# Performance work log

Hardware: AMD Instinct MI355X
Metric: run time of the kernel (lower is better)

## Reference

```python
import jax, jax.numpy as jnp
import numpy as np

EPS = 1e-07

def setup_inputs() -> dict:
    key = jax.random.key(0)
    k1, k2 = jax.random.split(key)
    B, C = 65536, 1000
    output = jax.random.normal(k1, (B, C), dtype=jnp.float32)
    target = jax.random.randint(k2, (B,), 0, C, dtype=jnp.int64)
    return {"output": output, "target": target}

def reference(output, target):
    B, C = output.shape
    # L2-normalize each row (p=2 norm over class dim) then softmax over classes
    norms = jnp.linalg.norm(output, axis=-1, keepdims=True) + EPS
    probs = jax.nn.softmax(output / norms, axis=1)  # [B, C]
    # per-class mean confidence [C]
    avg_conf = jnp.mean(probs, axis=0)
    # per-class empirical frequency [C] via one-hot-free bincount
    counts = jnp.zeros((C,), dtype=probs.dtype).at[target].add(1.0)
    avg_count = counts / B
    # mean absolute calibration gap over classes (scalar)
    return jnp.mean(jnp.abs(avg_conf - avg_count))
```

## Files before the change

kernel.cpp:

```cpp
#include <hip/hip_runtime.h>
#include <math.h>

#define TPB 512
#define NBLK 1024
#define CCLS 1000

__global__ __launch_bounds__(TPB, 8) void mdca_main(const float* __restrict__ X,
                                                    float* __restrict__ g_acc, int B) {
  __shared__ float sacc[1024];
  const int t = threadIdx.x;
  const int lane = t & 63;
  const int wid = blockIdx.x * (TPB / 64) + (t >> 6);
  const int nw = NBLK * (TPB / 64);
  const bool v3 = (lane < 58);

  for (int i = t; i < 1024; i += TPB) sacc[i] = 0.f;

  float acc[16];
  #pragma unroll
  for (int i = 0; i < 16; ++i) acc[i] = 0.f;

  const float4 Z = make_float4(0.f, 0.f, 0.f, 0.f);

  for (int r0 = wid; r0 < B; r0 += 2 * nw) {
    const int r1 = r0 + nw;
    const bool has1 = (r1 < B);

    const float4* b0 = reinterpret_cast<const float4*>(X + (size_t)r0 * CCLS);
    const float4* b1 = reinterpret_cast<const float4*>(X + (size_t)(has1 ? r1 : r0) * CCLS);

    float4 a0 = b0[lane],       a1 = b0[64 + lane];
    float4 a2 = b0[128 + lane], a3 = v3 ? b0[192 + lane] : Z;
    float4 c0 = b1[lane],       c1 = b1[64 + lane];
    float4 c2 = b1[128 + lane], c3 = v3 ? b1[192 + lane] : Z;

    float ss0 = a0.x*a0.x + a0.y*a0.y + a0.z*a0.z + a0.w*a0.w
              + a1.x*a1.x + a1.y*a1.y + a1.z*a1.z + a1.w*a1.w
              + a2.x*a2.x + a2.y*a2.y + a2.z*a2.z + a2.w*a2.w
              + a3.x*a3.x + a3.y*a3.y + a3.z*a3.z + a3.w*a3.w;
    float ss1 = c0.x*c0.x + c0.y*c0.y + c0.z*c0.z + c0.w*c0.w
              + c1.x*c1.x + c1.y*c1.y + c1.z*c1.z + c1.w*c1.w
              + c2.x*c2.x + c2.y*c2.y + c2.z*c2.z + c2.w*c2.w
              + c3.x*c3.x + c3.y*c3.y + c3.z*c3.z + c3.w*c3.w;

    #pragma unroll
    for (int off = 1; off < 64; off <<= 1) {
      ss0 += __shfl_xor(ss0, off, 64);
      ss1 += __shfl_xor(ss1, off, 64);
    }

    const float inv0 = 1.0f / (sqrtf(ss0) + 1e-7f);
    const float inv1 = 1.0f / (sqrtf(ss1) + 1e-7f);

    float e0[16], e1[16];
    e0[0]=__expf(a0.x*inv0); e0[1]=__expf(a0.y*inv0); e0[2]=__expf(a0.z*inv0); e0[3]=__expf(a0.w*inv0);
    e0[4]=__expf(a1.x*inv0); e0[5]=__expf(a1.y*inv0); e0[6]=__expf(a1.z*inv0); e0[7]=__expf(a1.w*inv0);
    e0[8]=__expf(a2.x*inv0); e0[9]=__expf(a2.y*inv0); e0[10]=__expf(a2.z*inv0); e0[11]=__expf(a2.w*inv0);
    e1[0]=__expf(c0.x*inv1); e1[1]=__expf(c0.y*inv1); e1[2]=__expf(c0.z*inv1); e1[3]=__expf(c0.w*inv1);
    e1[4]=__expf(c1.x*inv1); e1[5]=__expf(c1.y*inv1); e1[6]=__expf(c1.z*inv1); e1[7]=__expf(c1.w*inv1);
    e1[8]=__expf(c2.x*inv1); e1[9]=__expf(c2.y*inv1); e1[10]=__expf(c2.z*inv1); e1[11]=__expf(c2.w*inv1);
    if (v3) {
      e0[12]=__expf(a3.x*inv0); e0[13]=__expf(a3.y*inv0); e0[14]=__expf(a3.z*inv0); e0[15]=__expf(a3.w*inv0);
      e1[12]=__expf(c3.x*inv1); e1[13]=__expf(c3.y*inv1); e1[14]=__expf(c3.z*inv1); e1[15]=__expf(c3.w*inv1);
    } else {
      e0[12]=e0[13]=e0[14]=e0[15]=0.f;
      e1[12]=e1[13]=e1[14]=e1[15]=0.f;
    }

    float es0 = 0.f, es1 = 0.f;
    #pragma unroll
    for (int i = 0; i < 16; ++i) { es0 += e0[i]; es1 += e1[i]; }
    #pragma unroll
    for (int off = 1; off < 64; off <<= 1) {
      es0 += __shfl_xor(es0, off, 64);
      es1 += __shfl_xor(es1, off, 64);
    }
    const float invS0 = 1.0f / es0;
    const float invS1 = has1 ? (1.0f / es1) : 0.f;

    #pragma unroll
    for (int i = 0; i < 16; ++i) acc[i] += e0[i] * invS0 + e1[i] * invS1;
  }

  __syncthreads();
  #pragma unroll
  for (int k = 0; k < 4; ++k)
    #pragma unroll
    for (int j = 0; j < 4; ++j)
      atomicAdd(&sacc[k * 256 + lane * 4 + j], acc[k * 4 + j]);
  __syncthreads();
  #pragma unroll
  for (int j = 0; j < 2; ++j) {
    int c = t * 2 + j;
    if (c < CCLS) atomicAdd(&g_acc[c], sacc[c]);
  }
}

__global__ __launch_bounds__(256) void mdca_count(const int* __restrict__ tgt,
                                                  float* __restrict__ g_cnt, int B) {
  __shared__ int scnt[CCLS];
  for (int i = threadIdx.x; i < CCLS; i += 256) scnt[i] = 0;
  __syncthreads();
  for (int i = blockIdx.x * 256 + threadIdx.x; i < B; i += gridDim.x * 256)
    atomicAdd(&scnt[tgt[i]], 1);
  __syncthreads();
  for (int i = threadIdx.x; i < CCLS; i += 256) {
    int v = scnt[i];
    if (v) atomicAdd(&g_cnt[i], (float)v);
  }
}

__global__ __launch_bounds__(256) void mdca_final(const float* __restrict__ g_acc,
                                                  const float* __restrict__ g_cnt,
                                                  float* __restrict__ out, int B) {
  __shared__ float s_r[4];
  int t = threadIdx.x;
  float invB = 1.0f / (float)B;
  float s = 0.f;
  for (int c = t; c < CCLS; c += 256)
    s += fabsf((g_acc[c] - g_cnt[c]) * invB);
  #pragma unroll
  for (int off = 32; off > 0; off >>= 1) s += __shfl_down(s, off, 64);
  if ((t & 63) == 0) s_r[t >> 6] = s;
  __syncthreads();
  if (t == 0) out[0] = (s_r[0] + s_r[1] + s_r[2] + s_r[3]) / (float)CCLS;
}

extern "C" void kernel_launch(void* const* d_in, const int* in_sizes, int n_in,
                              void* d_out, int out_size, void* d_ws, size_t ws_size,
                              hipStream_t stream) {
  const float* X = (const float*)d_in[0];
  const int* tgt = (const int*)d_in[1];
  const int B = in_sizes[1];

  float* g_acc = (float*)d_ws;
  float* g_cnt = g_acc + 1024;

  hipMemsetAsync(d_ws, 0, 2048 * sizeof(float), stream);

  mdca_main<<<NBLK, TPB, 0, stream>>>(X, g_acc, B);
  mdca_count<<<32, 256, 0, stream>>>(tgt, g_cnt, B);
  mdca_final<<<1, 256, 0, stream>>>(g_acc, g_cnt, (float*)d_out, B);
}
```

Before: 406.9 us.

## Replace global float atomics with per-block partials and parallel final reduction

```diff
diff --git a/kernel.cpp b/kernel.cpp
--- a/kernel.cpp
+++ b/kernel.cpp
@@ -6,7 +6,7 @@
 #define CCLS 1000
 
 __global__ __launch_bounds__(TPB, 8) void mdca_main(const float* __restrict__ X,
-                                                    float* __restrict__ g_acc, int B) {
+                                                    float* __restrict__ part, int B) {
   __shared__ float sacc[1024];
   const int t = threadIdx.x;
   const int lane = t & 63;
@@ -52,24 +52,20 @@
     const float inv0 = 1.0f / (sqrtf(ss0) + 1e-7f);
     const float inv1 = 1.0f / (sqrtf(ss1) + 1e-7f);
 
-    float e0[16], e1[16];
-    e0[0]=__expf(a0.x*inv0); e0[1]=__expf(a0.y*inv0); e0[2]=__expf(a0.z*inv0); e0[3]=__expf(a0.w*inv0);
-    e0[4]=__expf(a1.x*inv0); e0[5]=__expf(a1.y*inv0); e0[6]=__expf(a1.z*inv0); e0[7]=__expf(a1.w*inv0);
-    e0[8]=__expf(a2.x*inv0); e0[9]=__expf(a2.y*inv0); e0[10]=__expf(a2.z*inv0); e0[11]=__expf(a2.w*inv0);
-    e1[0]=__expf(c0.x*inv1); e1[1]=__expf(c0.y*inv1); e1[2]=__expf(c0.z*inv1); e1[3]=__expf(c0.w*inv1);
-    e1[4]=__expf(c1.x*inv1); e1[5]=__expf(c1.y*inv1); e1[6]=__expf(c1.z*inv1); e1[7]=__expf(c1.w*inv1);
-    e1[8]=__expf(c2.x*inv1); e1[9]=__expf(c2.y*inv1); e1[10]=__expf(c2.z*inv1); e1[11]=__expf(c2.w*inv1);
-    if (v3) {
-      e0[12]=__expf(a3.x*inv0); e0[13]=__expf(a3.y*inv0); e0[14]=__expf(a3.z*inv0); e0[15]=__expf(a3.w*inv0);
-      e1[12]=__expf(c3.x*inv1); e1[13]=__expf(c3.y*inv1); e1[14]=__expf(c3.z*inv1); e1[15]=__expf(c3.w*inv1);
-    } else {
-      e0[12]=e0[13]=e0[14]=e0[15]=0.f;
-      e1[12]=e1[13]=e1[14]=e1[15]=0.f;
-    }
+    a0.x=__expf(a0.x*inv0); a0.y=__expf(a0.y*inv0); a0.z=__expf(a0.z*inv0); a0.w=__expf(a0.w*inv0);
+    a1.x=__expf(a1.x*inv0); a1.y=__expf(a1.y*inv0); a1.z=__expf(a1.z*inv0); a1.w=__expf(a1.w*inv0);
+    a2.x=__expf(a2.x*inv0); a2.y=__expf(a2.y*inv0); a2.z=__expf(a2.z*inv0); a2.w=__expf(a2.w*inv0);
+    a3.x=__expf(a3.x*inv0); a3.y=__expf(a3.y*inv0); a3.z=__expf(a3.z*inv0); a3.w=__expf(a3.w*inv0);
+    c0.x=__expf(c0.x*inv1); c0.y=__expf(c0.y*inv1); c0.z=__expf(c0.z*inv1); c0.w=__expf(c0.w*inv1);
+    c1.x=__expf(c1.x*inv1); c1.y=__expf(c1.y*inv1); c1.z=__expf(c1.z*inv1); c1.w=__expf(c1.w*inv1);
+    c2.x=__expf(c2.x*inv1); c2.y=__expf(c2.y*inv1); c2.z=__expf(c2.z*inv1); c2.w=__expf(c2.w*inv1);
+    c3.x=__expf(c3.x*inv1); c3.y=__expf(c3.y*inv1); c3.z=__expf(c3.z*inv1); c3.w=__expf(c3.w*inv1);
+    if (!v3) { a3 = Z; c3 = Z; }
 
-    float es0 = 0.f, es1 = 0.f;
-    #pragma unroll
-    for (int i = 0; i < 16; ++i) { es0 += e0[i]; es1 += e1[i]; }
+    float es0 = a0.x+a0.y+a0.z+a0.w + a1.x+a1.y+a1.z+a1.w
+              + a2.x+a2.y+a2.z+a2.w + a3.x+a3.y+a3.z+a3.w;
+    float es1 = c0.x+c0.y+c0.z+c0.w + c1.x+c1.y+c1.z+c1.w
+              + c2.x+c2.y+c2.z+c2.w + c3.x+c3.y+c3.z+c3.w;
     #pragma unroll
     for (int off = 1; off < 64; off <<= 1) {
       es0 += __shfl_xor(es0, off, 64);
@@ -78,8 +74,14 @@
     const float invS0 = 1.0f / es0;
     const float invS1 = has1 ? (1.0f / es1) : 0.f;
 
-    #pragma unroll
-    for (int i = 0; i < 16; ++i) acc[i] += e0[i] * invS0 + e1[i] * invS1;
+    acc[0]  += a0.x*invS0 + c0.x*invS1;  acc[1]  += a0.y*invS0 + c0.y*invS1;
+    acc[2]  += a0.z*invS0 + c0.z*invS1;  acc[3]  += a0.w*invS0 + c0.w*invS1;
+    acc[4]  += a1.x*invS0 + c1.x*invS1;  acc[5]  += a1.y*invS0 + c1.y*invS1;
+    acc[6]  += a1.z*invS0 + c1.z*invS1;  acc[7]  += a1.w*invS0 + c1.w*invS1;
+    acc[8]  += a2.x*invS0 + c2.x*invS1;  acc[9]  += a2.y*invS0 + c2.y*invS1;
+    acc[10] += a2.z*invS0 + c2.z*invS1;  acc[11] += a2.w*invS0 + c2.w*invS1;
+    acc[12] += a3.x*invS0 + c3.x*invS1;  acc[13] += a3.y*invS0 + c3.y*invS1;
+    acc[14] += a3.z*invS0 + c3.z*invS1;  acc[15] += a3.w*invS0 + c3.w*invS1;
   }
 
   __syncthreads();
@@ -89,10 +91,9 @@
     for (int j = 0; j < 4; ++j)
       atomicAdd(&sacc[k * 256 + lane * 4 + j], acc[k * 4 + j]);
   __syncthreads();
-  #pragma unroll
-  for (int j = 0; j < 2; ++j) {
-    int c = t * 2 + j;
-    if (c < CCLS) atomicAdd(&g_acc[c], sacc[c]);
+  if (t < 256) {
+    float4 v = *reinterpret_cast<float4*>(&sacc[t * 4]);
+    *reinterpret_cast<float4*>(&part[(size_t)blockIdx.x * 1024 + t * 4]) = v;
   }
 }
 
@@ -110,20 +111,25 @@
   }
 }
 
-__global__ __launch_bounds__(256) void mdca_final(const float* __restrict__ g_acc,
-                                                  const float* __restrict__ g_cnt,
-                                                  float* __restrict__ out, int B) {
-  __shared__ float s_r[4];
-  int t = threadIdx.x;
-  float invB = 1.0f / (float)B;
+__global__ __launch_bounds__(64) void mdca_final(const float* __restrict__ part,
+                                                 const float* __restrict__ g_cnt,
+                                                 float* __restrict__ out, int B) {
+  const int c = blockIdx.x * 64 + threadIdx.x;
   float s = 0.f;
-  for (int c = t; c < CCLS; c += 256)
-    s += fabsf((g_acc[c] - g_cnt[c]) * invB);
+  if (c < CCLS) {
+    float p0 = 0.f, p1 = 0.f, p2 = 0.f, p3 = 0.f;
+    for (int b = 0; b < NBLK; b += 4) {
+      p0 += part[(size_t)(b    ) * 1024 + c];
+      p1 += part[(size_t)(b + 1) * 1024 + c];
+      p2 += part[(size_t)(b + 2) * 1024 + c];
+      p3 += part[(size_t)(b + 3) * 1024 + c];
+    }
+    s = fabsf((p0 + p1 + p2 + p3) - g_cnt[c]);
+  }
   #pragma unroll
-  for (int off = 32; off > 0; off >>= 1) s += __shfl_down(s, off, 64);
-  if ((t & 63) == 0) s_r[t >> 6] = s;
-  __syncthreads();
-  if (t == 0) out[0] = (s_r[0] + s_r[1] + s_r[2] + s_r[3]) / (float)CCLS;
+  for (int off = 1; off < 64; off <<= 1) s += __shfl_xor(s, off, 64);
+  if (threadIdx.x == 0)
+    atomicAdd(out, s / ((float)B * (float)CCLS));
 }
 
 extern "C" void kernel_launch(void* const* d_in, const int* in_sizes, int n_in,
@@ -133,12 +139,13 @@
   const int* tgt = (const int*)d_in[1];
   const int B = in_sizes[1];
 
-  float* g_acc = (float*)d_ws;
-  float* g_cnt = g_acc + 1024;
+  float* g_cnt = (float*)d_ws;
+  float* part  = (float*)((char*)d_ws + 16384);
 
-  hipMemsetAsync(d_ws, 0, 2048 * sizeof(float), stream);
+  hipMemsetAsync(g_cnt, 0, 1024 * sizeof(float), stream);
+  hipMemsetAsync(d_out, 0, out_size * sizeof(float), stream);
 
-  mdca_main<<<NBLK, TPB, 0, stream>>>(X, g_acc, B);
   mdca_count<<<32, 256, 0, stream>>>(tgt, g_cnt, B);
-  mdca_final<<<1, 256, 0, stream>>>(g_acc, g_cnt, (float*)d_out, B);
+  mdca_main<<<NBLK, TPB, 0, stream>>>(X, part, B);
+  mdca_final<<<(CCLS + 63) / 64, 64, 0, stream>>>(part, g_cnt, (float*)d_out, B);
 }
```

New measurement: 518.0 us. 1.27x slower.

## Prefetch next row pair into registers and halve block size

Applied to the files above, without the earlier changes.

```diff
diff --git a/kernel.cpp b/kernel.cpp
--- a/kernel.cpp
+++ b/kernel.cpp
@@ -1,11 +1,24 @@
 #include <hip/hip_runtime.h>
 #include <math.h>
 
-#define TPB 512
+#define TPB 256
 #define NBLK 1024
 #define CCLS 1000
 
-__global__ __launch_bounds__(TPB, 8) void mdca_main(const float* __restrict__ X,
+
+#define LOADP(R, x0, x1, x2, x3, y0, y1, y2, y3)                                   \
+  {                                                                                \
+    const int _r1 = (R) + nw;                                                      \
+    const float4* _b0 = reinterpret_cast<const float4*>(X + (size_t)(R) * CCLS);   \
+    const float4* _b1 =                                                            \
+        reinterpret_cast<const float4*>(X + (size_t)(_r1 < B ? _r1 : (R)) * CCLS); \
+    x0 = _b0[lane];      x1 = _b0[64 + lane];                                      \
+    x2 = _b0[128 + lane]; x3 = v3 ? _b0[192 + lane] : Z;                           \
+    y0 = _b1[lane];      y1 = _b1[64 + lane];                                      \
+    y2 = _b1[128 + lane]; y3 = v3 ? _b1[192 + lane] : Z;                           \
+  }
+
+__global__ __launch_bounds__(TPB, 4) void mdca_main(const float* __restrict__ X,
                                                     float* __restrict__ g_acc, int B) {
   __shared__ float sacc[1024];
   const int t = threadIdx.x;
@@ -22,17 +35,16 @@
 
   const float4 Z = make_float4(0.f, 0.f, 0.f, 0.f);
 
-  for (int r0 = wid; r0 < B; r0 += 2 * nw) {
-    const int r1 = r0 + nw;
-    const bool has1 = (r1 < B);
+  float4 a0, a1, a2, a3, c0, c1, c2, c3;
+  int r0 = wid;
+  if (r0 < B) LOADP(r0, a0, a1, a2, a3, c0, c1, c2, c3);
 
-    const float4* b0 = reinterpret_cast<const float4*>(X + (size_t)r0 * CCLS);
-    const float4* b1 = reinterpret_cast<const float4*>(X + (size_t)(has1 ? r1 : r0) * CCLS);
+  while (r0 < B) {
+    const int rn = r0 + 2 * nw;
+    float4 na0 = Z, na1 = Z, na2 = Z, na3 = Z, nc0 = Z, nc1 = Z, nc2 = Z, nc3 = Z;
+    if (rn < B) LOADP(rn, na0, na1, na2, na3, nc0, nc1, nc2, nc3);
 
-    float4 a0 = b0[lane],       a1 = b0[64 + lane];
-    float4 a2 = b0[128 + lane], a3 = v3 ? b0[192 + lane] : Z;
-    float4 c0 = b1[lane],       c1 = b1[64 + lane];
-    float4 c2 = b1[128 + lane], c3 = v3 ? b1[192 + lane] : Z;
+    const bool has1 = (r0 + nw) < B;
 
     float ss0 = a0.x*a0.x + a0.y*a0.y + a0.z*a0.z + a0.w*a0.w
               + a1.x*a1.x + a1.y*a1.y + a1.z*a1.z + a1.w*a1.w
@@ -52,24 +64,20 @@
     const float inv0 = 1.0f / (sqrtf(ss0) + 1e-7f);
     const float inv1 = 1.0f / (sqrtf(ss1) + 1e-7f);
 
-    float e0[16], e1[16];
-    e0[0]=__expf(a0.x*inv0); e0[1]=__expf(a0.y*inv0); e0[2]=__expf(a0.z*inv0); e0[3]=__expf(a0.w*inv0);
-    e0[4]=__expf(a1.x*inv0); e0[5]=__expf(a1.y*inv0); e0[6]=__expf(a1.z*inv0); e0[7]=__expf(a1.w*inv0);
-    e0[8]=__expf(a2.x*inv0); e0[9]=__expf(a2.y*inv0); e0[10]=__expf(a2.z*inv0); e0[11]=__expf(a2.w*inv0);
-    e1[0]=__expf(c0.x*inv1); e1[1]=__expf(c0.y*inv1); e1[2]=__expf(c0.z*inv1); e1[3]=__expf(c0.w*inv1);
-    e1[4]=__expf(c1.x*inv1); e1[5]=__expf(c1.y*inv1); e1[6]=__expf(c1.z*inv1); e1[7]=__expf(c1.w*inv1);
-    e1[8]=__expf(c2.x*inv1); e1[9]=__expf(c2.y*inv1); e1[10]=__expf(c2.z*inv1); e1[11]=__expf(c2.w*inv1);
-    if (v3) {
-      e0[12]=__expf(a3.x*inv0); e0[13]=__expf(a3.y*inv0); e0[14]=__expf(a3.z*inv0); e0[15]=__expf(a3.w*inv0);
-      e1[12]=__expf(c3.x*inv1); e1[13]=__expf(c3.y*inv1); e1[14]=__expf(c3.z*inv1); e1[15]=__expf(c3.w*inv1);
-    } else {
-      e0[12]=e0[13]=e0[14]=e0[15]=0.f;
-      e1[12]=e1[13]=e1[14]=e1[15]=0.f;
-    }
+    a0.x=__expf(a0.x*inv0); a0.y=__expf(a0.y*inv0); a0.z=__expf(a0.z*inv0); a0.w=__expf(a0.w*inv0);
+    a1.x=__expf(a1.x*inv0); a1.y=__expf(a1.y*inv0); a1.z=__expf(a1.z*inv0); a1.w=__expf(a1.w*inv0);
+    a2.x=__expf(a2.x*inv0); a2.y=__expf(a2.y*inv0); a2.z=__expf(a2.z*inv0); a2.w=__expf(a2.w*inv0);
+    a3.x=__expf(a3.x*inv0); a3.y=__expf(a3.y*inv0); a3.z=__expf(a3.z*inv0); a3.w=__expf(a3.w*inv0);
+    c0.x=__expf(c0.x*inv1); c0.y=__expf(c0.y*inv1); c0.z=__expf(c0.z*inv1); c0.w=__expf(c0.w*inv1);
+    c1.x=__expf(c1.x*inv1); c1.y=__expf(c1.y*inv1); c1.z=__expf(c1.z*inv1); c1.w=__expf(c1.w*inv1);
+    c2.x=__expf(c2.x*inv1); c2.y=__expf(c2.y*inv1); c2.z=__expf(c2.z*inv1); c2.w=__expf(c2.w*inv1);
+    c3.x=__expf(c3.x*inv1); c3.y=__expf(c3.y*inv1); c3.z=__expf(c3.z*inv1); c3.w=__expf(c3.w*inv1);
+    if (!v3) { a3 = Z; c3 = Z; }
 
-    float es0 = 0.f, es1 = 0.f;
-    #pragma unroll
-    for (int i = 0; i < 16; ++i) { es0 += e0[i]; es1 += e1[i]; }
+    float es0 = a0.x+a0.y+a0.z+a0.w + a1.x+a1.y+a1.z+a1.w
+              + a2.x+a2.y+a2.z+a2.w + a3.x+a3.y+a3.z+a3.w;
+    float es1 = c0.x+c0.y+c0.z+c0.w + c1.x+c1.y+c1.z+c1.w
+              + c2.x+c2.y+c2.z+c2.w + c3.x+c3.y+c3.z+c3.w;
     #pragma unroll
     for (int off = 1; off < 64; off <<= 1) {
       es0 += __shfl_xor(es0, off, 64);
@@ -78,8 +86,18 @@
     const float invS0 = 1.0f / es0;
     const float invS1 = has1 ? (1.0f / es1) : 0.f;
 
-    #pragma unroll
-    for (int i = 0; i < 16; ++i) acc[i] += e0[i] * invS0 + e1[i] * invS1;
+    acc[0]  += a0.x*invS0 + c0.x*invS1;  acc[1]  += a0.y*invS0 + c0.y*invS1;
+    acc[2]  += a0.z*invS0 + c0.z*invS1;  acc[3]  += a0.w*invS0 + c0.w*invS1;
+    acc[4]  += a1.x*invS0 + c1.x*invS1;  acc[5]  += a1.y*invS0 + c1.y*invS1;
+    acc[6]  += a1.z*invS0 + c1.z*invS1;  acc[7]  += a1.w*invS0 + c1.w*invS1;
+    acc[8]  += a2.x*invS0 + c2.x*invS1;  acc[9]  += a2.y*invS0 + c2.y*invS1;
+    acc[10] += a2.z*invS0 + c2.z*invS1;  acc[11] += a2.w*invS0 + c2.w*invS1;
+    acc[12] += a3.x*invS0 + c3.x*invS1;  acc[13] += a3.y*invS0 + c3.y*invS1;
+    acc[14] += a3.z*invS0 + c3.z*invS1;  acc[15] += a3.w*invS0 + c3.w*invS1;
+
+    a0 = na0; a1 = na1; a2 = na2; a3 = na3;
+    c0 = nc0; c1 = nc1; c2 = nc2; c3 = nc3;
+    r0 = rn;
   }
 
   __syncthreads();
@@ -90,8 +108,8 @@
       atomicAdd(&sacc[k * 256 + lane * 4 + j], acc[k * 4 + j]);
   __syncthreads();
   #pragma unroll
-  for (int j = 0; j < 2; ++j) {
-    int c = t * 2 + j;
+  for (int j = 0; j < 4; ++j) {
+    int c = t * 4 + j;
     if (c < CCLS) atomicAdd(&g_acc[c], sacc[c]);
   }
 }
@@ -138,7 +156,7 @@
 
   hipMemsetAsync(d_ws, 0, 2048 * sizeof(float), stream);
 
+  mdca_count<<<32, 256, 0, stream>>>(tgt, g_cnt, B);
   mdca_main<<<NBLK, TPB, 0, stream>>>(X, g_acc, B);
-  mdca_count<<<32, 256, 0, stream>>>(tgt, g_cnt, B);
   mdca_final<<<1, 256, 0, stream>>>(g_acc, g_cnt, (float*)d_out, B);
 }
```

New measurement: 421.0 us. +3.5%, slower.
